# Optimization experiments

Hardware: AMD Instinct MI355X
Metric: run time of the kernel (lower is better)

## Reference

```python
import jax, jax.numpy as jnp
import numpy as np

D = 512
K = 14            # 13 anomaly classes + 1 normal
NORMAL_IDX = K - 1
ALPHA = 0.2       # PLG alpha
THETA = 0.55      # PLG threshold
EPS = 1e-8


def _minmax(x, axis):
    mn = jnp.min(x, axis=axis, keepdims=True)
    mx = jnp.max(x, axis=axis, keepdims=True)
    return (x - mn) / (mx - mn + EPS)


def setup_inputs() -> dict:
    key = jax.random.key(0)
    k1, k2, k3, k4, k5 = jax.random.split(key, 5)
    B_n, B_a, F = 16, 16, 4096
    normal_feats = jax.random.normal(k1, (B_n, F, D), dtype=jnp.float32)
    anomaly_feats = jax.random.normal(k2, (B_a, F, D), dtype=jnp.float32)
    anomaly_class_idx = jax.random.randint(k3, (B_a,), 0, K - 1)  # in [0, K-2]
    # learned text prompt embeddings (output of PromptTextEncoder, pre-normalization)
    T_emb = jax.random.normal(k4, (K, D), dtype=jnp.float32)
    # stand-in temporal scoring head (TCSAL replaced by linear head; see notes)
    w_score = jax.random.normal(k5, (D,), dtype=jnp.float32) / np.sqrt(D)
    b_score = jnp.zeros((), dtype=jnp.float32)
    return {"normal_feats": normal_feats, "anomaly_feats": anomaly_feats,
            "anomaly_class_idx": anomaly_class_idx, "T_emb": T_emb,
            "w_score": w_score, "b_score": b_score}


def reference(normal_feats, anomaly_feats, anomaly_class_idx, T_emb, w_score, b_score):
    B_a, F_a, _ = anomaly_feats.shape
    # L2-normalized text embeddings (K, D)
    T = T_emb / (jnp.linalg.norm(T_emb, axis=-1, keepdims=True) + EPS)
    T_anomaly = T[:NORMAL_IDX]          # (K-1, D)
    T_n = T[NORMAL_IDX]                 # (D,)  use_nvp=False -> T_n_enhanced = T_n
    T_n_enhanced = T_n

    # dense similarities
    S_nn = jnp.einsum('bfd,d->bf', normal_feats, T_n_enhanced)      # (B_n, F_n)
    phi_na = jnp.einsum('bfd,kd->bfk', normal_feats, T_anomaly)     # (B_n, F_n, K-1)
    S_an = jnp.einsum('bfd,d->bf', anomaly_feats, T_n_enhanced)     # (B_a, F_a)

    # per-sample true-class gather + matmul (vectorized: gather class vec then contract)
    T_true = T_anomaly[anomaly_class_idx]                            # (B_a, D)
    S_aa_true = jnp.einsum('bfd,bd->bf', anomaly_feats, T_true)      # (B_a, F_a)

    # 'other classes' similarities: exclude tau[b] per sample.
    # Since exactly one class is excluded, max_other = K-2 statically.
    phi_all = jnp.einsum('bfd,kd->bfk', anomaly_feats, T_anomaly)    # (B_a, F_a, K-1)
    j = jnp.arange(K - 2)                                            # (K-2,)
    other_idx = jnp.where(j[None, :] < anomaly_class_idx[:, None], j[None, :], j[None, :] + 1)  # (B_a, K-2)
    phi_aa_other = jnp.take_along_axis(
        phi_all, jnp.broadcast_to(other_idx[:, None, :], (B_a, F_a, K - 2)), axis=2)

    # pseudo-label generator (alpha-fused, normality-guided, thresholded)
    s_aa = _minmax(S_aa_true, axis=1)
    s_an = _minmax(S_an, axis=1)
    fused = (1.0 - ALPHA) * s_aa + ALPHA * (1.0 - s_an)
    pseudo_labels = (fused > THETA).astype(jnp.float32)

    # temporal scores (linear head stand-in for TCSAL)
    scores = jax.nn.sigmoid(jnp.einsum('bfd,d->bf', anomaly_feats, w_score) + b_score)

    S_aa_norm = _minmax(S_aa_true, axis=1)
    return (S_nn, phi_na, S_an, S_aa_true, phi_aa_other, S_aa_norm,
            pseudo_labels, scores, T_n_enhanced)
```

## Files before the change

kernel.cpp:

```cpp
#include <hip/hip_runtime.h>
#include <math.h>

#define D 512
#define K 14
#define EPS 1e-8f
#define NROWS 65536

#define O_SNN       0
#define O_PHINA     65536
#define O_SAN       917504
#define O_SAA       983040
#define O_PHIOTHER  1048576
#define O_SAANORM   1835008
#define O_PSEUDO    1900544
#define O_SCORES    1966080
#define O_TN        2031616

__device__ __forceinline__ float wave_sum(float v) {
    v += __shfl_xor(v, 1);
    v += __shfl_xor(v, 2);
    v += __shfl_xor(v, 4);
    v += __shfl_xor(v, 8);
    v += __shfl_xor(v, 16);
    v += __shfl_xor(v, 32);
    return v;
}
__device__ __forceinline__ float wave_min(float v) {
    v = fminf(v, __shfl_xor(v, 1));
    v = fminf(v, __shfl_xor(v, 2));
    v = fminf(v, __shfl_xor(v, 4));
    v = fminf(v, __shfl_xor(v, 8));
    v = fminf(v, __shfl_xor(v, 16));
    v = fminf(v, __shfl_xor(v, 32));
    return v;
}
__device__ __forceinline__ float wave_max(float v) {
    v = fmaxf(v, __shfl_xor(v, 1));
    v = fmaxf(v, __shfl_xor(v, 2));
    v = fmaxf(v, __shfl_xor(v, 4));
    v = fmaxf(v, __shfl_xor(v, 8));
    v = fmaxf(v, __shfl_xor(v, 16));
    v = fmaxf(v, __shfl_xor(v, 32));
    return v;
}

__global__ __launch_bounds__(960) void kprep(const float* __restrict__ T_emb,
                                             const float* __restrict__ w_score,
                                             float* __restrict__ W,
                                             float* __restrict__ tn_out) {
    int lane = threadIdx.x & 63;
    int w = threadIdx.x >> 6;
    float4* W4 = (float4*)W;
    if (w < K) {
        const float4* src = (const float4*)T_emb + w * 128;
        float4 a = src[lane];
        float4 b = src[64 + lane];
        float ss = a.x * a.x + a.y * a.y + a.z * a.z + a.w * a.w
                 + b.x * b.x + b.y * b.y + b.z * b.z + b.w * b.w;
        ss = wave_sum(ss);
        float inv = 1.0f / (sqrtf(ss) + EPS);
        float4 na = make_float4(a.x * inv, a.y * inv, a.z * inv, a.w * inv);
        float4 nb = make_float4(b.x * inv, b.y * inv, b.z * inv, b.w * inv);
        W4[w * 128 + lane] = na;
        W4[w * 128 + 64 + lane] = nb;
        if (w == K - 1) {
            float4* t4 = (float4*)tn_out;
            t4[lane] = na;
            t4[64 + lane] = nb;
        }
    } else {
        const float4* src = (const float4*)w_score;
        W4[14 * 128 + lane] = src[lane];
        W4[14 * 128 + 64 + lane] = src[64 + lane];
    }
}

template<int NK>
__global__ __launch_bounds__(256) void kdots(const float4* __restrict__ feats,
                                             const float4* __restrict__ W4,
                                             float* __restrict__ wsd) {
    const int lane = threadIdx.x & 63;
    const int wid  = threadIdx.x >> 6;
    const int row  = blockIdx.x * 256 + wid * 64 + lane;
    const int half = blockIdx.y;
    const int kb   = half * 64;

    const float4* fp = feats + (size_t)row * 128 + kb;
    const float4* tp = W4 + kb;

    float acc[NK];
#pragma unroll
    for (int j = 0; j < NK; j++) acc[j] = 0.0f;

#pragma unroll 4
    for (int s = 0; s < 64; s++) {
        float4 f = fp[s];
        int su = __builtin_amdgcn_readfirstlane(s);
#pragma unroll
        for (int j = 0; j < NK; j++) {
            float4 t = tp[j * 128 + su];
            acc[j] = fmaf(f.x, t.x, fmaf(f.y, t.y, fmaf(f.z, t.z, fmaf(f.w, t.w, acc[j]))));
        }
    }

    float4* o = (float4*)(wsd + ((size_t)half * NROWS + row) * 16);
    o[0] = make_float4(acc[0], acc[1], acc[2],  acc[3]);
    o[1] = make_float4(acc[4], acc[5], acc[6],  acc[7]);
    o[2] = make_float4(acc[8], acc[9], acc[10], acc[11]);
    o[3] = make_float4(acc[12], acc[13], (NK > 14) ? acc[14] : 0.0f, 0.0f);
}

__global__ __launch_bounds__(256) void kpostN(const float* __restrict__ wsd,
                                              float* __restrict__ S_nn,
                                              float* __restrict__ phi_na) {
    int i = blockIdx.x * 256 + threadIdx.x;
    int row = i >> 4, j = i & 15;
    float v = wsd[i] + wsd[NROWS * 16 + i];
    if (j < 13)       phi_na[row * 13 + j] = v;
    else if (j == 13) S_nn[row] = v;
}

__global__ __launch_bounds__(256) void kpostA(const float* __restrict__ wsd,
                                              const int* __restrict__ cls,
                                              const float* __restrict__ b_score,
                                              float* __restrict__ S_an,
                                              float* __restrict__ S_aa,
                                              float* __restrict__ phi_other,
                                              float* __restrict__ scores) {
    int i = blockIdx.x * 256 + threadIdx.x;
    int row = i >> 4, j = i & 15;
    float v = wsd[i] + wsd[NROWS * 16 + i];
    int ci = cls[row >> 12];
    if (j < 13) {
        if (j == ci) S_aa[row] = v;
        else         phi_other[row * 12 + ((j < ci) ? j : j - 1)] = v;
    } else if (j == 13) {
        S_an[row] = v;
    } else if (j == 14) {
        scores[row] = 1.0f / (1.0f + expf(-(v + b_score[0])));
    }
}

__global__ __launch_bounds__(256) void kminmax(const float* __restrict__ S_aa,
                                               const float* __restrict__ S_an,
                                               float* __restrict__ mm) {
    int b = blockIdx.x;
    int t = threadIdx.x;
    int lane = t & 63, wid = t >> 6;
    const float* pa = S_aa + b * 4096;
    const float* pn = S_an + b * 4096;
    float mnA = 1e30f, mxA = -1e30f, mnN = 1e30f, mxN = -1e30f;
    for (int i = t; i < 4096; i += 256) {
        float a = pa[i];
        float n = pn[i];
        mnA = fminf(mnA, a); mxA = fmaxf(mxA, a);
        mnN = fminf(mnN, n); mxN = fmaxf(mxN, n);
    }
    mnA = wave_min(mnA); mxA = wave_max(mxA);
    mnN = wave_min(mnN); mxN = wave_max(mxN);
    __shared__ float red[4][4];
    if (lane == 0) {
        red[wid][0] = mnA; red[wid][1] = mxA;
        red[wid][2] = mnN; red[wid][3] = mxN;
    }
    __syncthreads();
    if (t == 0) {
        float a0 = red[0][0], a1 = red[0][1], a2 = red[0][2], a3 = red[0][3];
        for (int w = 1; w < 4; w++) {
            a0 = fminf(a0, red[w][0]); a1 = fmaxf(a1, red[w][1]);
            a2 = fminf(a2, red[w][2]); a3 = fmaxf(a3, red[w][3]);
        }
        mm[b * 4 + 0] = a0; mm[b * 4 + 1] = a1;
        mm[b * 4 + 2] = a2; mm[b * 4 + 3] = a3;
    }
}

__global__ __launch_bounds__(256) void kfinal(const float* __restrict__ S_aa,
                                              const float* __restrict__ S_an,
                                              const float* __restrict__ mm,
                                              float* __restrict__ S_aa_norm,
                                              float* __restrict__ pseudo) {
    int i = blockIdx.x * 256 + threadIdx.x;
    if (i >= NROWS) return;
    int b = i >> 12;
    float mnA = mm[b * 4 + 0], mxA = mm[b * 4 + 1];
    float mnN = mm[b * 4 + 2], mxN = mm[b * 4 + 3];
    float s_aa = (S_aa[i] - mnA) / (mxA - mnA + EPS);
    float s_an = (S_an[i] - mnN) / (mxN - mnN + EPS);
    float fused = 0.8f * s_aa + 0.2f * (1.0f - s_an);
    pseudo[i] = fused > 0.55f ? 1.0f : 0.0f;
    S_aa_norm[i] = s_aa;
}

extern "C" void kernel_launch(void* const* d_in, const int* in_sizes, int n_in,
                              void* d_out, int out_size, void* d_ws, size_t ws_size,
                              hipStream_t stream) {
    const float* normal_feats  = (const float*)d_in[0];
    const float* anomaly_feats = (const float*)d_in[1];
    const int*   cls           = (const int*)d_in[2];
    const float* T_emb         = (const float*)d_in[3];
    const float* w_score       = (const float*)d_in[4];
    const float* b_score       = (const float*)d_in[5];
    float* out = (float*)d_out;

    float* W     = (float*)d_ws;
    float* mm    = (float*)d_ws + 8192;
    float* dotsN = (float*)d_ws + 8192 + 64;
    float* dotsA = dotsN + 2 * NROWS * 16;

    kprep<<<1, 960, 0, stream>>>(T_emb, w_score, W, out + O_TN);

    dim3 gdots(256, 2);
    kdots<14><<<gdots, 256, 0, stream>>>((const float4*)normal_feats,
                                         (const float4*)W, dotsN);
    kpostN<<<(NROWS * 16) / 256, 256, 0, stream>>>(dotsN, out + O_SNN, out + O_PHINA);

    kdots<15><<<gdots, 256, 0, stream>>>((const float4*)anomaly_feats,
                                         (const float4*)W, dotsA);
    kpostA<<<(NROWS * 16) / 256, 256, 0, stream>>>(dotsA, cls, b_score,
                                                   out + O_SAN, out + O_SAA,
                                                   out + O_PHIOTHER, out + O_SCORES);

    kminmax<<<16, 256, 0, stream>>>(out + O_SAA, out + O_SAN, mm);

    kfinal<<<256, 256, 0, stream>>>(out + O_SAA, out + O_SAN, mm,
                                    out + O_SAANORM, out + O_PSEUDO);
}
```

Before: 352.5 us.

## Fuse dot kernels with postprocessing, stage features via LDS, merge minmax and final

Merges the two dot-product kernels and their post-processing kernels into one launch over both inputs. Each block of 64 rows loads feature tiles with coalesced global reads into padded shared memory, and each of the four waves handles a quarter of D. Partial sums are reduced in LDS and scattered straight to the outputs, which removes the workspace round trip. The class-embedding matrix is stored interleaved (d-major, 15 classes contiguous) so the scalar loads are contiguous. The min/max and normalize kernels are merged into one per-batch kernel, at the cost of only 16 blocks doing the final pass.

```diff
diff --git a/kernel.cpp b/kernel.cpp
--- a/kernel.cpp
+++ b/kernel.cpp
@@ -17,40 +17,29 @@
 #define O_TN        2031616
 
 __device__ __forceinline__ float wave_sum(float v) {
-    v += __shfl_xor(v, 1);
-    v += __shfl_xor(v, 2);
-    v += __shfl_xor(v, 4);
-    v += __shfl_xor(v, 8);
-    v += __shfl_xor(v, 16);
-    v += __shfl_xor(v, 32);
+    v += __shfl_xor(v, 1);  v += __shfl_xor(v, 2);  v += __shfl_xor(v, 4);
+    v += __shfl_xor(v, 8);  v += __shfl_xor(v, 16); v += __shfl_xor(v, 32);
     return v;
 }
 __device__ __forceinline__ float wave_min(float v) {
-    v = fminf(v, __shfl_xor(v, 1));
-    v = fminf(v, __shfl_xor(v, 2));
-    v = fminf(v, __shfl_xor(v, 4));
-    v = fminf(v, __shfl_xor(v, 8));
-    v = fminf(v, __shfl_xor(v, 16));
-    v = fminf(v, __shfl_xor(v, 32));
+    v = fminf(v, __shfl_xor(v, 1));  v = fminf(v, __shfl_xor(v, 2));
+    v = fminf(v, __shfl_xor(v, 4));  v = fminf(v, __shfl_xor(v, 8));
+    v = fminf(v, __shfl_xor(v, 16)); v = fminf(v, __shfl_xor(v, 32));
     return v;
 }
 __device__ __forceinline__ float wave_max(float v) {
-    v = fmaxf(v, __shfl_xor(v, 1));
-    v = fmaxf(v, __shfl_xor(v, 2));
-    v = fmaxf(v, __shfl_xor(v, 4));
-    v = fmaxf(v, __shfl_xor(v, 8));
-    v = fmaxf(v, __shfl_xor(v, 16));
-    v = fmaxf(v, __shfl_xor(v, 32));
+    v = fmaxf(v, __shfl_xor(v, 1));  v = fmaxf(v, __shfl_xor(v, 2));
+    v = fmaxf(v, __shfl_xor(v, 4));  v = fmaxf(v, __shfl_xor(v, 8));
+    v = fmaxf(v, __shfl_xor(v, 16)); v = fmaxf(v, __shfl_xor(v, 32));
     return v;
 }
 
 __global__ __launch_bounds__(960) void kprep(const float* __restrict__ T_emb,
                                              const float* __restrict__ w_score,
-                                             float* __restrict__ W,
+                                             float4* __restrict__ Wt4,
                                              float* __restrict__ tn_out) {
     int lane = threadIdx.x & 63;
     int w = threadIdx.x >> 6;
-    float4* W4 = (float4*)W;
     if (w < K) {
         const float4* src = (const float4*)T_emb + w * 128;
         float4 a = src[lane];
@@ -61,8 +50,8 @@
         float inv = 1.0f / (sqrtf(ss) + EPS);
         float4 na = make_float4(a.x * inv, a.y * inv, a.z * inv, a.w * inv);
         float4 nb = make_float4(b.x * inv, b.y * inv, b.z * inv, b.w * inv);
-        W4[w * 128 + lane] = na;
-        W4[w * 128 + 64 + lane] = nb;
+        Wt4[lane * 15 + w] = na;
+        Wt4[(64 + lane) * 15 + w] = nb;
         if (w == K - 1) {
             float4* t4 = (float4*)tn_out;
             t4[lane] = na;
@@ -70,80 +59,101 @@
         }
     } else {
         const float4* src = (const float4*)w_score;
-        W4[14 * 128 + lane] = src[lane];
-        W4[14 * 128 + 64 + lane] = src[64 + lane];
-    }
-}
-
-template<int NK>
-__global__ __launch_bounds__(256) void kdots(const float4* __restrict__ feats,
-                                             const float4* __restrict__ W4,
-                                             float* __restrict__ wsd) {
-    const int lane = threadIdx.x & 63;
-    const int wid  = threadIdx.x >> 6;
-    const int row  = blockIdx.x * 256 + wid * 64 + lane;
-    const int half = blockIdx.y;
-    const int kb   = half * 64;
-
-    const float4* fp = feats + (size_t)row * 128 + kb;
-    const float4* tp = W4 + kb;
-
-    float acc[NK];
-#pragma unroll
-    for (int j = 0; j < NK; j++) acc[j] = 0.0f;
-
-#pragma unroll 4
-    for (int s = 0; s < 64; s++) {
-        float4 f = fp[s];
-        int su = __builtin_amdgcn_readfirstlane(s);
-#pragma unroll
-        for (int j = 0; j < NK; j++) {
-            float4 t = tp[j * 128 + su];
-            acc[j] = fmaf(f.x, t.x, fmaf(f.y, t.y, fmaf(f.z, t.z, fmaf(f.w, t.w, acc[j]))));
-        }
-    }
-
-    float4* o = (float4*)(wsd + ((size_t)half * NROWS + row) * 16);
-    o[0] = make_float4(acc[0], acc[1], acc[2],  acc[3]);
-    o[1] = make_float4(acc[4], acc[5], acc[6],  acc[7]);
-    o[2] = make_float4(acc[8], acc[9], acc[10], acc[11]);
-    o[3] = make_float4(acc[12], acc[13], (NK > 14) ? acc[14] : 0.0f, 0.0f);
-}
-
-__global__ __launch_bounds__(256) void kpostN(const float* __restrict__ wsd,
-                                              float* __restrict__ S_nn,
-                                              float* __restrict__ phi_na) {
-    int i = blockIdx.x * 256 + threadIdx.x;
-    int row = i >> 4, j = i & 15;
-    float v = wsd[i] + wsd[NROWS * 16 + i];
-    if (j < 13)       phi_na[row * 13 + j] = v;
-    else if (j == 13) S_nn[row] = v;
-}
-
-__global__ __launch_bounds__(256) void kpostA(const float* __restrict__ wsd,
-                                              const int* __restrict__ cls,
-                                              const float* __restrict__ b_score,
-                                              float* __restrict__ S_an,
-                                              float* __restrict__ S_aa,
-                                              float* __restrict__ phi_other,
-                                              float* __restrict__ scores) {
-    int i = blockIdx.x * 256 + threadIdx.x;
-    int row = i >> 4, j = i & 15;
-    float v = wsd[i] + wsd[NROWS * 16 + i];
-    int ci = cls[row >> 12];
-    if (j < 13) {
-        if (j == ci) S_aa[row] = v;
-        else         phi_other[row * 12 + ((j < ci) ? j : j - 1)] = v;
-    } else if (j == 13) {
-        S_an[row] = v;
-    } else if (j == 14) {
-        scores[row] = 1.0f / (1.0f + expf(-(v + b_score[0])));
-    }
-}
-
-__global__ __launch_bounds__(256) void kminmax(const float* __restrict__ S_aa,
-                                               const float* __restrict__ S_an,
-                                               float* __restrict__ mm) {
+        Wt4[lane * 15 + 14] = src[lane];
+        Wt4[(64 + lane) * 15 + 14] = src[64 + lane];
+    }
+}
+
+__global__ __launch_bounds__(256, 4) void kdots(const float4* __restrict__ nf4,
+                                                const float4* __restrict__ af4,
+                                                const float4* __restrict__ Wt4,
+                                                const int* __restrict__ cls,
+                                                const float* __restrict__ b_score,
+                                                float* __restrict__ S_nn,
+                                                float* __restrict__ phi_na,
+                                                float* __restrict__ S_an,
+                                                float* __restrict__ S_aa,
+                                                float* __restrict__ phi_other,
+                                                float* __restrict__ scores) {
+    __shared__ float smem[9216];
+    const int tid  = threadIdx.x;
+    const int l    = tid & 63;
+    const int w    = tid >> 6;
+    const int rbase = blockIdx.x * 64;
+    const bool anom = (blockIdx.y != 0);
+    const float4* feats4 = anom ? af4 : nf4;
+
+    float* sb = &smem[w * 2304];
+
+    const int sr = l >> 3;
+    const int sc = l & 7;
+    const float4* gbase = feats4 + (size_t)(rbase + sr) * 128 + w * 32 + sc;
+    const int wslot = sr * 9 + sc;
+
+    float4 g[8];
+#pragma unroll
+    for (int j = 0; j < 8; j++) g[j] = gbase[j * 1024];
+
+    float acc[15];
+#pragma unroll
+    for (int k = 0; k < 15; k++) acc[k] = 0.0f;
+
+#pragma unroll 1
+    for (int i = 0; i < 4; i++) {
+#pragma unroll
+        for (int j = 0; j < 8; j++)
+            *(float4*)&sb[j * 288 + wslot * 4] = g[j];
+        if (i < 3) {
+#pragma unroll
+            for (int j = 0; j < 8; j++) g[j] = gbase[j * 1024 + (i + 1) * 8];
+        }
+#pragma unroll
+        for (int s = 0; s < 8; s++) {
+            float4 f = *(const float4*)&sb[l * 36 + s * 4];
+            int su = __builtin_amdgcn_readfirstlane(w * 32 + i * 8 + s);
+#pragma unroll
+            for (int k = 0; k < 15; k++) {
+                float4 t = Wt4[su * 15 + k];
+                acc[k] = fmaf(f.x, t.x, fmaf(f.y, t.y,
+                          fmaf(f.z, t.z, fmaf(f.w, t.w, acc[k]))));
+            }
+        }
+    }
+
+    __syncthreads();
+#pragma unroll
+    for (int k = 0; k < 15; k++)
+        smem[w * 1088 + l * 17 + k] = acc[k];
+    __syncthreads();
+
+    const float bsc = b_score[0];
+    const int ci = anom ? cls[rbase >> 12] : 0;
+    for (int v = tid; v < 64 * 15; v += 256) {
+        int r = v / 15;
+        int j = v - r * 15;
+        float s = smem[r * 17 + j] + smem[1088 + r * 17 + j]
+                + smem[2176 + r * 17 + j] + smem[3264 + r * 17 + j];
+        int row = rbase + r;
+        if (!anom) {
+            if (j < 13)       phi_na[row * 13 + j] = s;
+            else if (j == 13) S_nn[row] = s;
+        } else {
+            if (j < 13) {
+                if (j == ci) S_aa[row] = s;
+                else         phi_other[row * 12 + ((j < ci) ? j : j - 1)] = s;
+            } else if (j == 13) {
+                S_an[row] = s;
+            } else {
+                scores[row] = 1.0f / (1.0f + expf(-(s + bsc)));
+            }
+        }
+    }
+}
+
+__global__ __launch_bounds__(256) void kbatch(const float* __restrict__ S_aa,
+                                              const float* __restrict__ S_an,
+                                              float* __restrict__ S_aa_norm,
+                                              float* __restrict__ pseudo) {
     int b = blockIdx.x;
     int t = threadIdx.x;
     int lane = t & 63, wid = t >> 6;
@@ -159,6 +169,7 @@
     mnA = wave_min(mnA); mxA = wave_max(mxA);
     mnN = wave_min(mnN); mxN = wave_max(mxN);
     __shared__ float red[4][4];
+    __shared__ float bc[4];
     if (lane == 0) {
         red[wid][0] = mnA; red[wid][1] = mxA;
         red[wid][2] = mnN; red[wid][3] = mxN;
@@ -166,30 +177,23 @@
     __syncthreads();
     if (t == 0) {
         float a0 = red[0][0], a1 = red[0][1], a2 = red[0][2], a3 = red[0][3];
-        for (int w = 1; w < 4; w++) {
-            a0 = fminf(a0, red[w][0]); a1 = fmaxf(a1, red[w][1]);
-            a2 = fminf(a2, red[w][2]); a3 = fmaxf(a3, red[w][3]);
-        }
-        mm[b * 4 + 0] = a0; mm[b * 4 + 1] = a1;
-        mm[b * 4 + 2] = a2; mm[b * 4 + 3] = a3;
-    }
-}
-
-__global__ __launch_bounds__(256) void kfinal(const float* __restrict__ S_aa,
-                                              const float* __restrict__ S_an,
-                                              const float* __restrict__ mm,
-                                              float* __restrict__ S_aa_norm,
-                                              float* __restrict__ pseudo) {
-    int i = blockIdx.x * 256 + threadIdx.x;
-    if (i >= NROWS) return;
-    int b = i >> 12;
-    float mnA = mm[b * 4 + 0], mxA = mm[b * 4 + 1];
-    float mnN = mm[b * 4 + 2], mxN = mm[b * 4 + 3];
-    float s_aa = (S_aa[i] - mnA) / (mxA - mnA + EPS);
-    float s_an = (S_an[i] - mnN) / (mxN - mnN + EPS);
-    float fused = 0.8f * s_aa + 0.2f * (1.0f - s_an);
-    pseudo[i] = fused > 0.55f ? 1.0f : 0.0f;
-    S_aa_norm[i] = s_aa;
+        for (int ww = 1; ww < 4; ww++) {
+            a0 = fminf(a0, red[ww][0]); a1 = fmaxf(a1, red[ww][1]);
+            a2 = fminf(a2, red[ww][2]); a3 = fmaxf(a3, red[ww][3]);
+        }
+        bc[0] = a0; bc[1] = a1; bc[2] = a2; bc[3] = a3;
+    }
+    __syncthreads();
+    float fmnA = bc[0], fmxA = bc[1], fmnN = bc[2], fmxN = bc[3];
+    float invA = 1.0f / (fmxA - fmnA + EPS);
+    float invN = 1.0f / (fmxN - fmnN + EPS);
+    for (int i = t; i < 4096; i += 256) {
+        float s_aa = (pa[i] - fmnA) * invA;
+        float s_an = (pn[i] - fmnN) * invN;
+        float fused = 0.8f * s_aa + 0.2f * (1.0f - s_an);
+        pseudo[b * 4096 + i] = fused > 0.55f ? 1.0f : 0.0f;
+        S_aa_norm[b * 4096 + i] = s_aa;
+    }
 }
 
 extern "C" void kernel_launch(void* const* d_in, const int* in_sizes, int n_in,
@@ -203,26 +207,18 @@
     const float* b_score       = (const float*)d_in[5];
     float* out = (float*)d_out;
 
-    float* W     = (float*)d_ws;
-    float* mm    = (float*)d_ws + 8192;
-    float* dotsN = (float*)d_ws + 8192 + 64;
-    float* dotsA = dotsN + 2 * NROWS * 16;
-
-    kprep<<<1, 960, 0, stream>>>(T_emb, w_score, W, out + O_TN);
-
-    dim3 gdots(256, 2);
-    kdots<14><<<gdots, 256, 0, stream>>>((const float4*)normal_feats,
-                                         (const float4*)W, dotsN);
-    kpostN<<<(NROWS * 16) / 256, 256, 0, stream>>>(dotsN, out + O_SNN, out + O_PHINA);
-
-    kdots<15><<<gdots, 256, 0, stream>>>((const float4*)anomaly_feats,
-                                         (const float4*)W, dotsA);
-    kpostA<<<(NROWS * 16) / 256, 256, 0, stream>>>(dotsA, cls, b_score,
-                                                   out + O_SAN, out + O_SAA,
-                                                   out + O_PHIOTHER, out + O_SCORES);
-
-    kminmax<<<16, 256, 0, stream>>>(out + O_SAA, out + O_SAN, mm);
-
-    kfinal<<<256, 256, 0, stream>>>(out + O_SAA, out + O_SAN, mm,
-                                    out + O_SAANORM, out + O_PSEUDO);
-}
+    float4* Wt4 = (float4*)d_ws;
+
+    kprep<<<1, 960, 0, stream>>>(T_emb, w_score, Wt4, out + O_TN);
+
+    dim3 gd(1024, 2);
+    kdots<<<gd, 256, 0, stream>>>((const float4*)normal_feats,
+                                  (const float4*)anomaly_feats,
+                                  Wt4, cls, b_score,
+                                  out + O_SNN, out + O_PHINA,
+                                  out + O_SAN, out + O_SAA,
+                                  out + O_PHIOTHER, out + O_SCORES);
+
+    kbatch<<<16, 256, 0, stream>>>(out + O_SAA, out + O_SAN,
+                                   out + O_SAANORM, out + O_PSEUDO);
+}
```

Result: no change. 346.6 us (-1.7%).
